# Kernel tuning notes

Hardware: AMD Instinct MI355X
Metric: run time of the kernel (lower is better)

The kernel has to match this reference:

```python
import jax, jax.numpy as jnp
import numpy as np

NUM_HEADS = 8
H_SCALE = 1000.0
WIND_THRESHOLD = 5.0


def setup_inputs() -> dict:
    key = jax.random.key(0)
    ks = jax.random.split(key, 8)
    B, N, C = 8, 1024, 256
    H = W = 64  # (H//2)*(W//2) == N
    x = jax.random.normal(ks[0], (B, N, C), dtype=jnp.float32)
    elevation = jax.random.uniform(ks[1], (B, N), dtype=jnp.float32)
    u_wind = jax.random.normal(ks[2], (B, H, W), dtype=jnp.float32)
    v_wind = jax.random.normal(ks[3], (B, H, W), dtype=jnp.float32)
    w_qkv = jax.random.normal(ks[4], (3 * C, C), dtype=jnp.float32) * (C ** -0.5)
    w_proj = jax.random.normal(ks[5], (C, C), dtype=jnp.float32) * (C ** -0.5)
    b_proj = jnp.zeros((C,), dtype=jnp.float32)
    alpha = jnp.float32(1.0)
    beta = jnp.float32(0.3)
    return {"x": x, "elevation": elevation, "u_wind": u_wind, "v_wind": v_wind,
            "w_qkv": w_qkv, "w_proj": w_proj, "b_proj": b_proj,
            "alpha": alpha, "beta": beta}


def _wind_strength(u_wind, v_wind):
    # 2x2 average pool of wind magnitude -> [B, N]
    B, H, W = u_wind.shape
    mag = jnp.sqrt(u_wind ** 2 + v_wind ** 2 + 1e-8)
    mag = mag.reshape(B, H // 2, 2, W // 2, 2).mean(axis=(2, 4))
    return mag.reshape(B, -1)


def _elevation_bias(elevation, u_wind, v_wind, alpha, beta):
    # elev_diff[b,i,j] = elev[b,j] - elev[b,i]
    elev_diff = elevation[:, None, :] - elevation[:, :, None]
    bias = -alpha * jax.nn.relu(elev_diff / H_SCALE)
    ws = _wind_strength(u_wind, v_wind)  # [B, N]
    wind_factor = jax.nn.sigmoid((ws[:, None, :] + ws[:, :, None]) * 0.5 - WIND_THRESHOLD)
    bias = bias * (1.0 - beta * wind_factor)
    return jnp.clip(bias, -10.0, 0.0)  # [B, N, N]


def reference(x, elevation, u_wind, v_wind, w_qkv, w_proj, b_proj, alpha, beta):
    B, N, C = x.shape
    hd = C // NUM_HEADS
    scale = hd ** -0.5
    qkv = (x @ w_qkv.T).reshape(B, N, 3, NUM_HEADS, hd)
    qkv = jnp.transpose(qkv, (2, 0, 3, 1, 4))  # [3, B, H, N, hd]
    q, k, v = qkv[0], qkv[1], qkv[2]
    scores = jnp.einsum('bhnd,bhmd->bhnm', q, k) * scale
    bias = _elevation_bias(elevation, u_wind, v_wind, alpha, beta)
    scores = scores + bias[:, None, :, :]
    attn = jax.nn.softmax(scores, axis=-1)
    out = jnp.einsum('bhnm,bhmd->bhnd', attn, v)
    out = jnp.transpose(out, (0, 2, 1, 3)).reshape(B, N, C)
    return out @ w_proj.T + b_proj
```

## Files before the change

kernel.cpp:

```cpp
#include <hip/hip_runtime.h>
#include <stdint.h>

typedef __attribute__((ext_vector_type(8))) short short8;
typedef __attribute__((ext_vector_type(8))) __bf16 bf16x8;
typedef __attribute__((ext_vector_type(2))) __bf16 bf16x2;
typedef __attribute__((ext_vector_type(4))) float f32x4;
typedef __attribute__((ext_vector_type(2))) unsigned int uint2_t;
typedef __attribute__((ext_vector_type(2))) float float2_t;

#define LOG2E 1.44269504f

__device__ __forceinline__ unsigned short f2bf(float f) {
  unsigned int u = __builtin_bit_cast(unsigned int, f);
  u += 0x7fffu + ((u >> 16) & 1u);
  return (unsigned short)(u >> 16);
}

__device__ __forceinline__ unsigned int pk2(float a, float b) {
  bf16x2 t;
  t[0] = (__bf16)a;
  t[1] = (__bf16)b;
  return __builtin_bit_cast(unsigned int, t);
}

__device__ __forceinline__ f32x4 mfma16(short8 a, short8 b, f32x4 c) {
  return __builtin_amdgcn_mfma_f32_16x16x32_bf16(
      __builtin_bit_cast(bf16x8, a), __builtin_bit_cast(bf16x8, b), c, 0, 0, 0);
}

__device__ __forceinline__ short8 ld8(const unsigned short* p) {
  return *reinterpret_cast<const short8*>(p);
}

__global__ __launch_bounds__(256) void k_prep(const float* __restrict__ wqkv,
                                              const float* __restrict__ wproj,
                                              const float* __restrict__ u,
                                              const float* __restrict__ v,
                                              const float* __restrict__ elev,
                                              const float* __restrict__ alphap,
                                              unsigned short* __restrict__ wqkv_bf,
                                              unsigned short* __restrict__ wproj_bf,
                                              float* __restrict__ esc,
                                              float* __restrict__ wsc) {
  int gx = blockIdx.x, t = threadIdx.x;
  if (gx < 768) {
    int i = gx * 256 + t;
    float s = (i < 256 * 256) ? (0.17677669529663687f * LOG2E) : 1.0f;
    wqkv_bf[i] = f2bf(wqkv[i] * s);
  } else if (gx < 1024) {
    int i = (gx - 768) * 256 + t;
    wproj_bf[i] = f2bf(wproj[i]);
  } else {
    int i = (gx - 1024) * 256 + t;
    int b = i >> 10, n = i & 1023;
    int ph = n >> 5, pw = n & 31;
    const float* ub = u + b * 4096;
    const float* vb = v + b * 4096;
    float s = 0.f;
#pragma unroll
    for (int dy = 0; dy < 2; ++dy)
#pragma unroll
      for (int dx = 0; dx < 2; ++dx) {
        int idx = (2 * ph + dy) * 64 + (2 * pw + dx);
        float uu = ub[idx], vv = vb[idx];
        s += sqrtf(uu * uu + vv * vv + 1e-8f);
      }
    wsc[i] = s * (0.25f * 0.5f * LOG2E);
    esc[i] = elev[i] * (alphap[0] * 1e-3f * LOG2E);
  }
}

__global__ __launch_bounds__(256, 8) void k_qkv(const float* __restrict__ x,
                                                const unsigned short* __restrict__ wq_bf,
                                                unsigned short* __restrict__ qb,
                                                unsigned short* __restrict__ kb,
                                                unsigned short* __restrict__ vT) {
  __shared__ unsigned short xs[32][264];
  const int tid = threadIdx.x;
  const int w = tid >> 6, lane = tid & 63;
  const int c = lane & 15, g = lane >> 4;
  const int wm = w & 1, wn = w >> 1;
  const int m0 = blockIdx.y * 32;
  const int n0 = blockIdx.x * 192 + wn * 96;
#pragma unroll
  for (int i = 0; i < 8; ++i) {
    int idx = i * 1024 + tid * 4;
    int row = idx >> 8, col = idx & 255;
    f32x4 vv = *reinterpret_cast<const f32x4*>(x + (size_t)(m0 + row) * 256 + col);
    uint2_t hh = {pk2(vv[0], vv[1]), pk2(vv[2], vv[3])};
    *reinterpret_cast<uint2_t*>(&xs[row][col]) = hh;
  }
  __syncthreads();
  f32x4 acc[6] = {};
#pragma unroll
  for (int k0 = 0; k0 < 256; k0 += 32) {
    short8 af = ld8(&xs[wm * 16 + c][k0 + g * 8]);
#pragma unroll
    for (int nb = 0; nb < 6; ++nb) {
      short8 bf = ld8(wq_bf + (size_t)(n0 + nb * 16 + c) * 256 + k0 + g * 8);
      acc[nb] = mfma16(af, bf, acc[nb]);
    }
  }
#pragma unroll
  for (int nb = 0; nb < 6; ++nb) {
    int col = n0 + nb * 16 + c;
    int s = col >> 8, rem = col & 255;
    int h = rem >> 5, d = rem & 31;
    int nrow0 = m0 + wm * 16 + g * 4;
    int b = nrow0 >> 10, nn = nrow0 & 1023;
    size_t bh = (size_t)(b * 8 + h);
    if (s == 2) {
      uint2_t pk = {pk2(acc[nb][0], acc[nb][1]), pk2(acc[nb][2], acc[nb][3])};
      *reinterpret_cast<uint2_t*>(vT + (bh * 32 + d) * 1024 + nn) = pk;
    } else {
      unsigned short* dst = (s == 0) ? qb : kb;
#pragma unroll
      for (int r = 0; r < 4; ++r) {
        bf16x2 one;
        one[0] = (__bf16)acc[nb][r];
        dst[(bh * 1024 + nn + r) * 32 + d] = __builtin_bit_cast(unsigned short, one[0]);
      }
    }
  }
}

__global__ __launch_bounds__(256, 4) void k_attn(const unsigned short* __restrict__ qb,
                                                 const unsigned short* __restrict__ kb,
                                                 const unsigned short* __restrict__ vT,
                                                 const float* __restrict__ esc,
                                                 const float* __restrict__ wsc,
                                                 const float* __restrict__ betap,
                                                 float* __restrict__ o_part,
                                                 float* __restrict__ ml_part) {
  __shared__ float bias_lds[32][72];
  __shared__ unsigned short p_lds[4][32][72];
  const int tid = threadIdx.x;
  const int w = tid >> 6, lane = tid & 63;
  const int c = lane & 15, g = lane >> 4;
  const int q0 = blockIdx.x * 32, b = blockIdx.y;
  const int hg = blockIdx.z & 1, sp = blockIdx.z >> 1;
  const int h = hg * 4 + w;
  const size_t bh = (size_t)(b * 8 + h);
  const int kvbase = sp * 512;
  const float beta = betap[0];

  const int sqr = tid >> 3, skv = (tid & 7) * 8;
  const float* ebs = esc + b * 1024;
  const float* wbs = wsc + b * 1024;
  const float eisc = ebs[q0 + sqr];
  const float Kw = 7.2134752f - wbs[q0 + sqr];

  auto bias_elem = [&](float ej, float wj) -> float {
    float d = fmaxf(ej - eisc, 0.f);
    float e2 = __builtin_amdgcn_exp2f(Kw - wj);
    float sig = __builtin_amdgcn_rcpf(1.0f + e2);
    float bb = d * beta * sig - d;
    return fminf(fmaxf(bb, -14.4269504f), 0.f);
  };
  auto stage_bias = [&](int kv0) {
    f32x4 ej0 = *reinterpret_cast<const f32x4*>(ebs + kv0 + skv);
    f32x4 ej1 = *reinterpret_cast<const f32x4*>(ebs + kv0 + skv + 4);
    f32x4 wj0 = *reinterpret_cast<const f32x4*>(wbs + kv0 + skv);
    f32x4 wj1 = *reinterpret_cast<const f32x4*>(wbs + kv0 + skv + 4);
    f32x4 o0, o1;
#pragma unroll
    for (int j = 0; j < 4; ++j) {
      o0[j] = bias_elem(ej0[j], wj0[j]);
      o1[j] = bias_elem(ej1[j], wj1[j]);
    }
    *reinterpret_cast<f32x4*>(&bias_lds[sqr][skv]) = o0;
    *reinterpret_cast<f32x4*>(&bias_lds[sqr][skv + 4]) = o1;
  };

  stage_bias(kvbase);

  short8 qf[2];
#pragma unroll
  for (int qs = 0; qs < 2; ++qs)
    qf[qs] = ld8(qb + (bh * 1024 + q0 + qs * 16 + c) * 32 + g * 8);

  f32x4 oacc[2][2] = {};
  float mold[2] = {-1e30f, -1e30f};
  float lrow[2] = {0.f, 0.f};
  __syncthreads();

  for (int t8 = 0; t8 < 8; ++t8) {
    const int kv0 = kvbase + t8 * 64;

    short8 kf[4];
#pragma unroll
    for (int t = 0; t < 4; ++t)
      kf[t] = ld8(kb + (bh * 1024 + kv0 + t * 16 + c) * 32 + g * 8);

#pragma unroll
    for (int qs = 0; qs < 2; ++qs) {
      f32x4 s[4];
#pragma unroll
      for (int t = 0; t < 4; ++t) {
        f32x4 bc = *reinterpret_cast<const f32x4*>(&bias_lds[qs * 16 + c][t * 16 + 4 * g]);
        s[t] = mfma16(kf[t], qf[qs], bc);
      }
      float m16 = fmaxf(fmaxf(fmaxf(s[0][0], s[0][1]), fmaxf(s[0][2], s[0][3])),
                        fmaxf(fmaxf(s[1][0], s[1][1]), fmaxf(s[1][2], s[1][3])));
      m16 = fmaxf(m16, fmaxf(fmaxf(fmaxf(s[2][0], s[2][1]), fmaxf(s[2][2], s[2][3])),
                             fmaxf(fmaxf(s[3][0], s[3][1]), fmaxf(s[3][2], s[3][3]))));
      m16 = fmaxf(m16, __shfl_xor(m16, 16));
      m16 = fmaxf(m16, __shfl_xor(m16, 32));
      if (!__all(m16 <= mold[qs] + 11.0f)) {
        float mn = fmaxf(mold[qs], m16);
        float corr = __builtin_amdgcn_exp2f(mold[qs] - mn);
        mold[qs] = mn;
        lrow[qs] *= corr;
        oacc[qs][0] *= corr;
        oacc[qs][1] *= corr;
      }
      float ps = 0.f;
#pragma unroll
      for (int t = 0; t < 4; ++t) {
        float e0 = __builtin_amdgcn_exp2f(s[t][0] - mold[qs]);
        float e1 = __builtin_amdgcn_exp2f(s[t][1] - mold[qs]);
        float e2 = __builtin_amdgcn_exp2f(s[t][2] - mold[qs]);
        float e3 = __builtin_amdgcn_exp2f(s[t][3] - mold[qs]);
        ps += (e0 + e1) + (e2 + e3);
        uint2_t pkw = {pk2(e0, e1), pk2(e2, e3)};
        *reinterpret_cast<uint2_t*>(&p_lds[w][qs * 16 + c][t * 16 + 4 * g]) = pkw;
      }
      ps += __shfl_xor(ps, 16);
      ps += __shfl_xor(ps, 32);
      lrow[qs] += ps;
    }

    __syncthreads();
    if (t8 < 7) stage_bias(kv0 + 64);

#pragma unroll
    for (int t2 = 0; t2 < 2; ++t2) {
      short8 pf[2];
#pragma unroll
      for (int qs = 0; qs < 2; ++qs)
        pf[qs] = ld8(&p_lds[w][qs * 16 + c][t2 * 32 + g * 8]);
#pragma unroll
      for (int hs = 0; hs < 2; ++hs) {
        short8 vf = ld8(vT + (bh * 32 + hs * 16 + c) * 1024 + kv0 + t2 * 32 + g * 8);
#pragma unroll
        for (int qs = 0; qs < 2; ++qs)
          oacc[qs][hs] = mfma16(vf, pf[qs], oacc[qs][hs]);
      }
    }

    __syncthreads();
  }

#pragma unroll
  for (int qs = 0; qs < 2; ++qs) {
    size_t qrow = ((size_t)sp * 64 + bh) * 1024 + q0 + qs * 16 + c;
#pragma unroll
    for (int hs = 0; hs < 2; ++hs)
      *reinterpret_cast<f32x4*>(o_part + qrow * 32 + hs * 16 + 4 * g) = oacc[qs][hs];
    if (g == 0) {
      float2_t ml = {mold[qs], lrow[qs]};
      *reinterpret_cast<float2_t*>(ml_part + qrow * 2) = ml;
    }
  }
}

__global__ __launch_bounds__(256, 2) void k_proj(const float* __restrict__ o_part,
                                                 const float* __restrict__ ml_part,
                                                 const unsigned short* __restrict__ wp_bf,
                                                 const float* __restrict__ bproj,
                                                 float* __restrict__ out) {
  __shared__ unsigned short xs[32][264];
  const int tid = threadIdx.x;
  const int w = tid >> 6, lane = tid & 63;
  const int c = lane & 15, g = lane >> 4;
  const int wm = w & 1, wn = w >> 1;
  const int m0 = blockIdx.x * 32;
  const int b = m0 >> 10, q0 = m0 & 1023;

  const int qq = tid >> 3, d0 = (tid & 7) * 4;
#pragma unroll
  for (int h = 0; h < 8; ++h) {
    size_t r0 = ((size_t)(b * 8 + h) * 1024 + q0 + qq);
    size_t r1 = r0 + (size_t)64 * 1024;
    f32x4 o0 = *reinterpret_cast<const f32x4*>(o_part + r0 * 32 + d0);
    f32x4 o1 = *reinterpret_cast<const f32x4*>(o_part + r1 * 32 + d0);
    float2_t ml0 = *reinterpret_cast<const float2_t*>(ml_part + r0 * 2);
    float2_t ml1 = *reinterpret_cast<const float2_t*>(ml_part + r1 * 2);
    float mm = fmaxf(ml0[0], ml1[0]);
    float a0 = __builtin_amdgcn_exp2f(ml0[0] - mm);
    float a1 = __builtin_amdgcn_exp2f(ml1[0] - mm);
    float inv = 1.0f / (a0 * ml0[1] + a1 * ml1[1]);
    f32x4 r;
#pragma unroll
    for (int j = 0; j < 4; ++j) r[j] = (o0[j] * a0 + o1[j] * a1) * inv;
    uint2_t hh = {pk2(r[0], r[1]), pk2(r[2], r[3])};
    *reinterpret_cast<uint2_t*>(&xs[qq][h * 32 + d0]) = hh;
  }
  __syncthreads();

  f32x4 acc[8] = {};
#pragma unroll
  for (int k0 = 0; k0 < 256; k0 += 32) {
    short8 af = ld8(&xs[wm * 16 + c][k0 + g * 8]);
#pragma unroll
    for (int nb = 0; nb < 8; ++nb) {
      short8 bf = ld8(wp_bf + (size_t)(wn * 128 + nb * 16 + c) * 256 + k0 + g * 8);
      acc[nb] = mfma16(af, bf, acc[nb]);
    }
  }
#pragma unroll
  for (int nb = 0; nb < 8; ++nb) {
    int col = wn * 128 + nb * 16 + c;
    float bv = bproj[col];
#pragma unroll
    for (int r = 0; r < 4; ++r) {
      int row = m0 + wm * 16 + g * 4 + r;
      out[(size_t)row * 256 + col] = acc[nb][r] + bv;
    }
  }
}

extern "C" void kernel_launch(void* const* d_in, const int* in_sizes, int n_in,
                              void* d_out, int out_size, void* d_ws, size_t ws_size,
                              hipStream_t stream) {
  const float* x = (const float*)d_in[0];
  const float* elev = (const float*)d_in[1];
  const float* uw = (const float*)d_in[2];
  const float* vw = (const float*)d_in[3];
  const float* wqkv = (const float*)d_in[4];
  const float* wproj = (const float*)d_in[5];
  const float* bproj = (const float*)d_in[6];
  const float* alpha = (const float*)d_in[7];
  const float* beta = (const float*)d_in[8];
  float* out = (float*)d_out;

  char* p = (char*)d_ws;
  auto alloc = [&](size_t bytes) {
    char* r = p;
    p += (bytes + 255) & ~(size_t)255;
    return r;
  };
  float* esc = (float*)alloc(8192 * 4);
  float* wsc = (float*)alloc(8192 * 4);
  unsigned short* wqkv_bf = (unsigned short*)alloc((size_t)768 * 256 * 2);
  unsigned short* wproj_bf = (unsigned short*)alloc((size_t)256 * 256 * 2);
  unsigned short* qb = (unsigned short*)alloc((size_t)2097152 * 2);
  unsigned short* kb = (unsigned short*)alloc((size_t)2097152 * 2);
  unsigned short* vT = (unsigned short*)alloc((size_t)2097152 * 2);
  float* o_part = (float*)alloc((size_t)2 * 2097152 * 4);
  float* ml_part = (float*)alloc((size_t)2 * 65536 * 2 * 4);

  k_prep<<<dim3(1056), dim3(256), 0, stream>>>(wqkv, wproj, uw, vw, elev, alpha,
                                               wqkv_bf, wproj_bf, esc, wsc);
  k_qkv<<<dim3(4, 256), dim3(256), 0, stream>>>(x, wqkv_bf, qb, kb, vT);
  k_attn<<<dim3(32, 8, 4), dim3(256), 0, stream>>>(qb, kb, vT, esc, wsc, beta, o_part, ml_part);
  k_proj<<<dim3(256), dim3(256), 0, stream>>>(o_part, ml_part, wproj_bf, bproj, out);
}
```

Baseline: 153.2 us.

## Factor wind sigmoid exp into per-token products and retile projection kernel

```diff
diff --git a/kernel.cpp b/kernel.cpp
--- a/kernel.cpp
+++ b/kernel.cpp
@@ -41,7 +41,7 @@
                                               unsigned short* __restrict__ wqkv_bf,
                                               unsigned short* __restrict__ wproj_bf,
                                               float* __restrict__ esc,
-                                              float* __restrict__ wsc) {
+                                              float* __restrict__ pw) {
   int gx = blockIdx.x, t = threadIdx.x;
   if (gx < 768) {
     int i = gx * 256 + t;
@@ -53,7 +53,7 @@
   } else {
     int i = (gx - 1024) * 256 + t;
     int b = i >> 10, n = i & 1023;
-    int ph = n >> 5, pw = n & 31;
+    int ph = n >> 5, pw_ = n & 31;
     const float* ub = u + b * 4096;
     const float* vb = v + b * 4096;
     float s = 0.f;
@@ -61,11 +61,12 @@
     for (int dy = 0; dy < 2; ++dy)
 #pragma unroll
       for (int dx = 0; dx < 2; ++dx) {
-        int idx = (2 * ph + dy) * 64 + (2 * pw + dx);
+        int idx = (2 * ph + dy) * 64 + (2 * pw_ + dx);
         float uu = ub[idx], vv = vb[idx];
         s += sqrtf(uu * uu + vv * vv + 1e-8f);
       }
-    wsc[i] = s * (0.25f * 0.5f * LOG2E);
+    float wsc = s * (0.25f * 0.5f * LOG2E);
+    pw[i] = __builtin_amdgcn_exp2f(-wsc);
     esc[i] = elev[i] * (alphap[0] * 1e-3f * LOG2E);
   }
 }
@@ -128,7 +129,7 @@
                                                  const unsigned short* __restrict__ kb,
                                                  const unsigned short* __restrict__ vT,
                                                  const float* __restrict__ esc,
-                                                 const float* __restrict__ wsc,
+                                                 const float* __restrict__ pw,
                                                  const float* __restrict__ betap,
                                                  float* __restrict__ o_part,
                                                  float* __restrict__ ml_part) {
@@ -146,13 +147,13 @@
 
   const int sqr = tid >> 3, skv = (tid & 7) * 8;
   const float* ebs = esc + b * 1024;
-  const float* wbs = wsc + b * 1024;
+  const float* pbs = pw + b * 1024;
   const float eisc = ebs[q0 + sqr];
-  const float Kw = 7.2134752f - wbs[q0 + sqr];
-
-  auto bias_elem = [&](float ej, float wj) -> float {
+  const float pwi5 = 148.4131591f * pbs[q0 + sqr];
+
+  auto bias_elem = [&](float ej, float pj) -> float {
     float d = fmaxf(ej - eisc, 0.f);
-    float e2 = __builtin_amdgcn_exp2f(Kw - wj);
+    float e2 = pwi5 * pj;
     float sig = __builtin_amdgcn_rcpf(1.0f + e2);
     float bb = d * beta * sig - d;
     return fminf(fmaxf(bb, -14.4269504f), 0.f);
@@ -160,13 +161,13 @@
   auto stage_bias = [&](int kv0) {
     f32x4 ej0 = *reinterpret_cast<const f32x4*>(ebs + kv0 + skv);
     f32x4 ej1 = *reinterpret_cast<const f32x4*>(ebs + kv0 + skv + 4);
-    f32x4 wj0 = *reinterpret_cast<const f32x4*>(wbs + kv0 + skv);
-    f32x4 wj1 = *reinterpret_cast<const f32x4*>(wbs + kv0 + skv + 4);
+    f32x4 pj0 = *reinterpret_cast<const f32x4*>(pbs + kv0 + skv);
+    f32x4 pj1 = *reinterpret_cast<const f32x4*>(pbs + kv0 + skv + 4);
     f32x4 o0, o1;
 #pragma unroll
     for (int j = 0; j < 4; ++j) {
-      o0[j] = bias_elem(ej0[j], wj0[j]);
-      o1[j] = bias_elem(ej1[j], wj1[j]);
+      o0[j] = bias_elem(ej0[j], pj0[j]);
+      o1[j] = bias_elem(ej1[j], pj1[j]);
     }
     *reinterpret_cast<f32x4*>(&bias_lds[sqr][skv]) = o0;
     *reinterpret_cast<f32x4*>(&bias_lds[sqr][skv + 4]) = o1;
@@ -264,57 +265,63 @@
   }
 }
 
-__global__ __launch_bounds__(256, 2) void k_proj(const float* __restrict__ o_part,
+__global__ __launch_bounds__(256, 4) void k_proj(const float* __restrict__ o_part,
                                                  const float* __restrict__ ml_part,
                                                  const unsigned short* __restrict__ wp_bf,
                                                  const float* __restrict__ bproj,
                                                  float* __restrict__ out) {
-  __shared__ unsigned short xs[32][264];
+  __shared__ unsigned short xs[16][264];
+  __shared__ float cl[8][16][2];
   const int tid = threadIdx.x;
   const int w = tid >> 6, lane = tid & 63;
   const int c = lane & 15, g = lane >> 4;
-  const int wm = w & 1, wn = w >> 1;
-  const int m0 = blockIdx.x * 32;
+  const int m0 = blockIdx.x * 16;
   const int b = m0 >> 10, q0 = m0 & 1023;
 
-  const int qq = tid >> 3, d0 = (tid & 7) * 4;
-#pragma unroll
-  for (int h = 0; h < 8; ++h) {
-    size_t r0 = ((size_t)(b * 8 + h) * 1024 + q0 + qq);
-    size_t r1 = r0 + (size_t)64 * 1024;
-    f32x4 o0 = *reinterpret_cast<const f32x4*>(o_part + r0 * 32 + d0);
-    f32x4 o1 = *reinterpret_cast<const f32x4*>(o_part + r1 * 32 + d0);
-    float2_t ml0 = *reinterpret_cast<const float2_t*>(ml_part + r0 * 2);
-    float2_t ml1 = *reinterpret_cast<const float2_t*>(ml_part + r1 * 2);
+  if (tid < 128) {
+    int h = tid >> 4, row = tid & 15;
+    size_t base = ((size_t)(b * 8 + h)) * 1024 + q0 + row;
+    float2_t ml0 = *reinterpret_cast<const float2_t*>(ml_part + base * 2);
+    float2_t ml1 = *reinterpret_cast<const float2_t*>(ml_part + (base + (size_t)65536) * 2);
     float mm = fmaxf(ml0[0], ml1[0]);
     float a0 = __builtin_amdgcn_exp2f(ml0[0] - mm);
     float a1 = __builtin_amdgcn_exp2f(ml1[0] - mm);
     float inv = 1.0f / (a0 * ml0[1] + a1 * ml1[1]);
-    f32x4 r;
-#pragma unroll
-    for (int j = 0; j < 4; ++j) r[j] = (o0[j] * a0 + o1[j] * a1) * inv;
-    uint2_t hh = {pk2(r[0], r[1]), pk2(r[2], r[3])};
-    *reinterpret_cast<uint2_t*>(&xs[qq][h * 32 + d0]) = hh;
+    cl[h][row][0] = a0 * inv;
+    cl[h][row][1] = a1 * inv;
   }
   __syncthreads();
 
-  f32x4 acc[8] = {};
+  const int rr = tid >> 4, cs = (tid & 15) * 2;
+#pragma unroll
+  for (int h = 0; h < 8; ++h) {
+    size_t base = ((size_t)(b * 8 + h)) * 1024 + q0 + rr;
+    float2_t o0 = *reinterpret_cast<const float2_t*>(o_part + base * 32 + cs);
+    float2_t o1 = *reinterpret_cast<const float2_t*>(o_part + (base + (size_t)65536) * 32 + cs);
+    float c0 = cl[h][rr][0], c1 = cl[h][rr][1];
+    float r0 = o0[0] * c0 + o1[0] * c1;
+    float r1 = o0[1] * c0 + o1[1] * c1;
+    *reinterpret_cast<unsigned int*>(&xs[rr][h * 32 + cs]) = pk2(r0, r1);
+  }
+  __syncthreads();
+
+  f32x4 acc[4] = {};
 #pragma unroll
   for (int k0 = 0; k0 < 256; k0 += 32) {
-    short8 af = ld8(&xs[wm * 16 + c][k0 + g * 8]);
-#pragma unroll
-    for (int nb = 0; nb < 8; ++nb) {
-      short8 bf = ld8(wp_bf + (size_t)(wn * 128 + nb * 16 + c) * 256 + k0 + g * 8);
+    short8 af = ld8(&xs[c][k0 + g * 8]);
+#pragma unroll
+    for (int nb = 0; nb < 4; ++nb) {
+      short8 bf = ld8(wp_bf + (size_t)(w * 64 + nb * 16 + c) * 256 + k0 + g * 8);
       acc[nb] = mfma16(af, bf, acc[nb]);
     }
   }
 #pragma unroll
-  for (int nb = 0; nb < 8; ++nb) {
-    int col = wn * 128 + nb * 16 + c;
+  for (int nb = 0; nb < 4; ++nb) {
+    int col = w * 64 + nb * 16 + c;
     float bv = bproj[col];
 #pragma unroll
     for (int r = 0; r < 4; ++r) {
-      int row = m0 + wm * 16 + g * 4 + r;
+      int row = m0 + g * 4 + r;
       out[(size_t)row * 256 + col] = acc[nb][r] + bv;
     }
   }
@@ -341,7 +348,7 @@
     return r;
   };
   float* esc = (float*)alloc(8192 * 4);
-  float* wsc = (float*)alloc(8192 * 4);
+  float* pw = (float*)alloc(8192 * 4);
   unsigned short* wqkv_bf = (unsigned short*)alloc((size_t)768 * 256 * 2);
   unsigned short* wproj_bf = (unsigned short*)alloc((size_t)256 * 256 * 2);
   unsigned short* qb = (unsigned short*)alloc((size_t)2097152 * 2);
@@ -351,8 +358,8 @@
   float* ml_part = (float*)alloc((size_t)2 * 65536 * 2 * 4);
 
   k_prep<<<dim3(1056), dim3(256), 0, stream>>>(wqkv, wproj, uw, vw, elev, alpha,
-                                               wqkv_bf, wproj_bf, esc, wsc);
+                                               wqkv_bf, wproj_bf, esc, pw);
   k_qkv<<<dim3(4, 256), dim3(256), 0, stream>>>(x, wqkv_bf, qb, kb, vT);
-  k_attn<<<dim3(32, 8, 4), dim3(256), 0, stream>>>(qb, kb, vT, esc, wsc, beta, o_part, ml_part);
-  k_proj<<<dim3(256), dim3(256), 0, stream>>>(o_part, ml_part, wproj_bf, bproj, out);
-}
+  k_attn<<<dim3(32, 8, 4), dim3(256), 0, stream>>>(qb, kb, vT, esc, pw, beta, o_part, ml_part);
+  k_proj<<<dim3(512), dim3(256), 0, stream>>>(o_part, ml_part, wproj_bf, bproj, out);
+}
```

Result: no change. 153.2 us (-0.0%).
